# Kernel optimization log

Hardware: AMD Instinct MI355X
Metric: run time of the kernel (lower is better)

Reference implementation:

```python
import jax, jax.numpy as jnp
import numpy as np

N = 8192      # source grid points
M = 8192      # output grid points
NB = 16       # n_basis
WIDTH = 32    # int(n_basis * enhancement)
EPS = 1e-4
LOG2 = 0.6931471805599453


def log_cosh(x):
    a = jnp.abs(x)
    return a + jnp.log1p(jnp.exp(-2.0 * a)) - LOG2


def setup_inputs() -> dict:
    key = jax.random.key(0)
    ks = jax.random.split(key, 9)
    rho = jax.random.uniform(ks[0], (N,), minval=0.05, maxval=2.0)
    gamma = jax.random.uniform(ks[1], (N,), minval=0.01, maxval=1.0)
    coords = jax.random.normal(ks[2], (N, 3)) * 5.0
    weights = jax.random.uniform(ks[3], (N,), minval=0.0, maxval=0.1)
    out_coords = jax.random.normal(ks[4], (M, 3)) * 5.0
    # field_embed params: Linear(1 -> WIDTH), Linear(WIDTH -> NB)
    w1 = jax.random.normal(ks[5], (1, WIDTH)) * 1.0
    b1 = jax.random.normal(ks[6], (WIDTH,)) * 0.1
    w2 = jax.random.normal(ks[7], (WIDTH, NB)) / np.sqrt(WIDTH)
    b2 = jax.random.normal(ks[8], (NB,)) * 0.1
    return {"rho": rho, "gamma": gamma, "coords": coords, "weights": weights,
            "out_coords": out_coords, "w1": w1, "b1": b1, "w2": w2, "b2": b2}


def _field_embed(x, w1, b1, w2, b2):
    # x: (..., 1) -> (..., NB)
    return jnp.tanh(x @ w1 + b1) @ w2 + b2


def reference(rho, gamma, coords, weights, out_coords, w1, b1, w2, b2):
    # rescaled (reduced) density gradient s^2 = gamma / (4 (3 pi^2)^{2/3} rho^{8/3})
    s2 = gamma / (4.0 * (3.0 * jnp.pi ** 2) ** (2.0 / 3.0) * rho ** (8.0 / 3.0))
    x = jnp.log(s2 + EPS)[:, None]                     # (N, 1)
    exponent = log_cosh(_field_embed(x, w1, b1, w2, b2))  # (N, NB)
    heg_scale = log_cosh(_field_embed(jnp.zeros((1, 1), rho.dtype), w1, b1, w2, b2)) ** 1.5  # (1, NB)
    beta = jnp.pi * (rho[:, None] / 2.0) ** (2.0 / 3.0) * exponent  # (N, NB)
    wrho = weights * rho                                # (N,)

    # all-pairs squared distances (M, N), computed once
    d2 = (jnp.sum(out_coords ** 2, axis=1)[:, None]
          + jnp.sum(coords ** 2, axis=1)[None, :]
          - 2.0 * out_coords @ coords.T)
    d2 = jnp.maximum(d2, 0.0)

    # KeOps Genred: y[i, b] = sum_j exp(-beta[j, b] * d2[i, j]) * wrho[j]
    # scan over the (small, fixed) basis axis so only one (M, N) kernel slice lives at a time
    def body(carry, beta_b):                            # beta_b: (N,)
        yb = jnp.exp(-d2 * beta_b[None, :]) @ wrho      # (M,)
        return carry, yb

    _, ys = jax.lax.scan(body, 0, beta.T)               # (NB, M)
    return ys.T * heg_scale                             # (M, NB)
```

## Files before the change

kernel.cpp:

```cpp
#include <hip/hip_runtime.h>
#include <hip/hip_bf16.h>


#define N_PTS 8192
#define M_PTS 8192
#define NBASIS 16
#define WIDTH 32

__device__ __forceinline__ float exp2_hw(float x) { return __builtin_amdgcn_exp2f(x); }
__device__ __forceinline__ float log2_hw(float x) { return __builtin_amdgcn_logf(x); }

__device__ __forceinline__ float fast_tanh(float z) {
    float a = fabsf(z);
    float t = __expf(-2.0f * a);
    float r = (1.0f - t) / (1.0f + t);
    return copysignf(r, z);
}

__device__ __forceinline__ float log_cosh_f(float x) {
    float a = fabsf(x);
    return a + __logf(1.0f + __expf(-2.0f * a)) - 0.6931471805599453f;
}

__global__ __launch_bounds__(64)
void cg_prep(const float* __restrict__ rho,
             const float* __restrict__ gamma,
             const float* __restrict__ coords,
             const float* __restrict__ weights,
             const float* __restrict__ w1,
             const float* __restrict__ b1,
             const float* __restrict__ w2,
             const float* __restrict__ b2,
             float4* __restrict__ cw,
             float4* __restrict__ bnq,
             float* __restrict__ hegf)
{
    const float PI_F = 3.14159265358979323846f;
    const float LOG2E = 1.4426950408889634f;

    __shared__ float s_w1[WIDTH], s_b1[WIDTH], s_w2[WIDTH * NBASIS], s_b2[NBASIS];
    int t = threadIdx.x;
    if (t < WIDTH) { s_w1[t] = w1[t]; s_b1[t] = b1[t]; }
    if (t < NBASIS) s_b2[t] = b2[t];
    #pragma unroll
    for (int k = 0; k < 8; ++k) s_w2[t + 64 * k] = w2[t + 64 * k];
    __syncthreads();

    int j = blockIdx.x * 64 + t;
    {
        float r = rho[j];
        float g = gamma[j];
        const float c83 = 38.28312007948569f;
        float r83 = exp2_hw(2.6666666667f * log2_hw(r));
        float s2 = g / (c83 * r83);
        float x = __logf(s2 + 1e-4f);

        float emb[NBASIS];
        #pragma unroll
        for (int b = 0; b < NBASIS; ++b) emb[b] = s_b2[b];
        #pragma unroll 4
        for (int w = 0; w < WIDTH; ++w) {
            float h = fast_tanh(fmaf(x, s_w1[w], s_b1[w]));
            #pragma unroll
            for (int b = 0; b < NBASIS; ++b)
                emb[b] = fmaf(h, s_w2[w * NBASIS + b], emb[b]);
        }
        float pref = PI_F * exp2_hw(0.6666666667f * log2_hw(0.5f * r));
        float scale = -LOG2E * pref;
        #pragma unroll
        for (int q = 0; q < 4; ++q) {
            bnq[q * N_PTS + j] = make_float4(scale * log_cosh_f(emb[4 * q + 0]),
                                             scale * log_cosh_f(emb[4 * q + 1]),
                                             scale * log_cosh_f(emb[4 * q + 2]),
                                             scale * log_cosh_f(emb[4 * q + 3]));
        }

        cw[j] = make_float4(coords[j * 3 + 0],
                            coords[j * 3 + 1],
                            coords[j * 3 + 2],
                            weights[j] * r);
    }

    if (blockIdx.x == 0 && t == 0) {
        float emb0[NBASIS];
        #pragma unroll
        for (int b = 0; b < NBASIS; ++b) emb0[b] = s_b2[b];
        for (int w = 0; w < WIDTH; ++w) {
            float h = fast_tanh(s_b1[w]);
            #pragma unroll
            for (int b = 0; b < NBASIS; ++b)
                emb0[b] = fmaf(h, s_w2[w * NBASIS + b], emb0[b]);
        }
        #pragma unroll
        for (int b = 0; b < NBASIS; ++b) {
            float lc = fmaxf(log_cosh_f(emb0[b]), 0.0f);
            hegf[b] = lc * sqrtf(lc);
        }
    }
}

__global__ __launch_bounds__(256, 4)
void cg_pairs(const float* __restrict__ oc,
              const float4* __restrict__ cw,
              const float4* __restrict__ bnq,
              const float* __restrict__ hegf,
              float* __restrict__ out)
{
    int wid  = (blockIdx.x << 2) | (threadIdx.x >> 6);
    int lane = threadIdx.x & 63;
    int pair = wid >> 1;
    int half = wid & 1;
    int i0 = pair << 1;
    int i1 = i0 | 1;
    int jbase = half << 12;

    float ox0 = oc[i0 * 3 + 0], oy0 = oc[i0 * 3 + 1], oz0 = oc[i0 * 3 + 2];
    float ox1 = oc[i1 * 3 + 0], oy1 = oc[i1 * 3 + 1], oz1 = oc[i1 * 3 + 2];

    float acc0[NBASIS], acc1[NBASIS];
    #pragma unroll
    for (int b = 0; b < NBASIS; ++b) { acc0[b] = 0.0f; acc1[b] = 0.0f; }

    #pragma unroll 2
    for (int k = 0; k < 64; ++k) {
        int j = jbase + (k << 6) + lane;
        float4 c = cw[j];
        float dx0 = ox0 - c.x, dy0 = oy0 - c.y, dz0 = oz0 - c.z;
        float dx1 = ox1 - c.x, dy1 = oy1 - c.y, dz1 = oz1 - c.z;
        float d20 = fmaf(dx0, dx0, fmaf(dy0, dy0, dz0 * dz0));
        float d21 = fmaf(dx1, dx1, fmaf(dy1, dy1, dz1 * dz1));
        #pragma unroll
        for (int q = 0; q < 4; ++q) {
            float4 b4 = bnq[q * N_PTS + j];
            float e00 = exp2_hw(b4.x * d20);
            float e01 = exp2_hw(b4.y * d20);
            float e02 = exp2_hw(b4.z * d20);
            float e03 = exp2_hw(b4.w * d20);
            float e10 = exp2_hw(b4.x * d21);
            float e11 = exp2_hw(b4.y * d21);
            float e12 = exp2_hw(b4.z * d21);
            float e13 = exp2_hw(b4.w * d21);
            acc0[q * 4 + 0] = fmaf(e00, c.w, acc0[q * 4 + 0]);
            acc0[q * 4 + 1] = fmaf(e01, c.w, acc0[q * 4 + 1]);
            acc0[q * 4 + 2] = fmaf(e02, c.w, acc0[q * 4 + 2]);
            acc0[q * 4 + 3] = fmaf(e03, c.w, acc0[q * 4 + 3]);
            acc1[q * 4 + 0] = fmaf(e10, c.w, acc1[q * 4 + 0]);
            acc1[q * 4 + 1] = fmaf(e11, c.w, acc1[q * 4 + 1]);
            acc1[q * 4 + 2] = fmaf(e12, c.w, acc1[q * 4 + 2]);
            acc1[q * 4 + 3] = fmaf(e13, c.w, acc1[q * 4 + 3]);
        }
    }

    #pragma unroll
    for (int m = 1; m < 64; m <<= 1) {
        #pragma unroll
        for (int b = 0; b < NBASIS; ++b) {
            acc0[b] += __shfl_xor(acc0[b], m, 64);
            acc1[b] += __shfl_xor(acc1[b], m, 64);
        }
    }

    if (lane == 0) {
        #pragma unroll
        for (int b = 0; b < NBASIS; ++b) {
            float h = hegf[b];
            atomicAdd(&out[i0 * NBASIS + b], acc0[b] * h);
            atomicAdd(&out[i1 * NBASIS + b], acc1[b] * h);
        }
    }
}

extern "C" void kernel_launch(void* const* d_in, const int* in_sizes, int n_in,
                              void* d_out, int out_size, void* d_ws, size_t ws_size,
                              hipStream_t stream) {
    const float* rho        = (const float*)d_in[0];
    const float* gamma      = (const float*)d_in[1];
    const float* coords     = (const float*)d_in[2];
    const float* weights    = (const float*)d_in[3];
    const float* out_coords = (const float*)d_in[4];
    const float* w1         = (const float*)d_in[5];
    const float* b1         = (const float*)d_in[6];
    const float* w2         = (const float*)d_in[7];
    const float* b2         = (const float*)d_in[8];

    char* ws = (char*)d_ws;
    float4* cw   = (float4*)(ws);
    float4* bnq  = (float4*)(ws + (128 << 10));
    float*  hegf = (float*) (ws + (640 << 10));

    (void)hipMemsetAsync(d_out, 0, (size_t)M_PTS * NBASIS * sizeof(float), stream);

    cg_prep<<<N_PTS / 64, 64, 0, stream>>>(rho, gamma, coords, weights,
                                           w1, b1, w2, b2,
                                           cw, bnq, hegf);

    cg_pairs<<<M_PTS / 4, 256, 0, stream>>>(out_coords, cw, bnq, hegf,
                                            (float*)d_out);
}
```

Measured before the change: 235.0 us.

## Give each wave the full source range and vectorize pair math with packed floats

Each wave now covers all 8192 source points for its two output rows instead of splitting them across two waves. This lets the results be written with plain stores, so the atomics and the output memset go away. The distance, multiply and accumulate math uses two-wide float vectors so the compiler can emit packed FP32 instructions, while exp2 stays scalar. The grid is halved, which lowers wave-level parallelism (1024 blocks on the device) and doubles the serial loop length per wave.

Result: faster. 190.6 us (-18.9%).

```diff
diff --git a/kernel.cpp b/kernel.cpp
--- a/kernel.cpp
+++ b/kernel.cpp
@@ -6,6 +6,8 @@
 #define M_PTS 8192
 #define NBASIS 16
 #define WIDTH 32
+
+typedef float v2f __attribute__((ext_vector_type(2)));
 
 __device__ __forceinline__ float exp2_hw(float x) { return __builtin_amdgcn_exp2f(x); }
 __device__ __forceinline__ float log2_hw(float x) { return __builtin_amdgcn_logf(x); }
@@ -106,48 +108,42 @@
               const float* __restrict__ hegf,
               float* __restrict__ out)
 {
-    int wid  = (blockIdx.x << 2) | (threadIdx.x >> 6);
+    int wave = (blockIdx.x << 2) | (threadIdx.x >> 6);
     int lane = threadIdx.x & 63;
-    int pair = wid >> 1;
-    int half = wid & 1;
-    int i0 = pair << 1;
+    int i0 = wave << 1;
     int i1 = i0 | 1;
-    int jbase = half << 12;
 
-    float ox0 = oc[i0 * 3 + 0], oy0 = oc[i0 * 3 + 1], oz0 = oc[i0 * 3 + 2];
-    float ox1 = oc[i1 * 3 + 0], oy1 = oc[i1 * 3 + 1], oz1 = oc[i1 * 3 + 2];
+    v2f oxv = { oc[i0 * 3 + 0], oc[i1 * 3 + 0] };
+    v2f oyv = { oc[i0 * 3 + 1], oc[i1 * 3 + 1] };
+    v2f ozv = { oc[i0 * 3 + 2], oc[i1 * 3 + 2] };
 
-    float acc0[NBASIS], acc1[NBASIS];
+    v2f acc[NBASIS];
     #pragma unroll
-    for (int b = 0; b < NBASIS; ++b) { acc0[b] = 0.0f; acc1[b] = 0.0f; }
+    for (int b = 0; b < NBASIS; ++b) acc[b] = (v2f)0.0f;
 
     #pragma unroll 2
-    for (int k = 0; k < 64; ++k) {
-        int j = jbase + (k << 6) + lane;
+    for (int k = 0; k < N_PTS / 64; ++k) {
+        int j = (k << 6) | lane;
         float4 c = cw[j];
-        float dx0 = ox0 - c.x, dy0 = oy0 - c.y, dz0 = oz0 - c.z;
-        float dx1 = ox1 - c.x, dy1 = oy1 - c.y, dz1 = oz1 - c.z;
-        float d20 = fmaf(dx0, dx0, fmaf(dy0, dy0, dz0 * dz0));
-        float d21 = fmaf(dx1, dx1, fmaf(dy1, dy1, dz1 * dz1));
+        v2f dx = oxv - c.x;
+        v2f dy = oyv - c.y;
+        v2f dz = ozv - c.z;
+        v2f d2 = dx * dx + dy * dy + dz * dz;
         #pragma unroll
         for (int q = 0; q < 4; ++q) {
             float4 b4 = bnq[q * N_PTS + j];
-            float e00 = exp2_hw(b4.x * d20);
-            float e01 = exp2_hw(b4.y * d20);
-            float e02 = exp2_hw(b4.z * d20);
-            float e03 = exp2_hw(b4.w * d20);
-            float e10 = exp2_hw(b4.x * d21);
-            float e11 = exp2_hw(b4.y * d21);
-            float e12 = exp2_hw(b4.z * d21);
-            float e13 = exp2_hw(b4.w * d21);
-            acc0[q * 4 + 0] = fmaf(e00, c.w, acc0[q * 4 + 0]);
-            acc0[q * 4 + 1] = fmaf(e01, c.w, acc0[q * 4 + 1]);
-            acc0[q * 4 + 2] = fmaf(e02, c.w, acc0[q * 4 + 2]);
-            acc0[q * 4 + 3] = fmaf(e03, c.w, acc0[q * 4 + 3]);
-            acc1[q * 4 + 0] = fmaf(e10, c.w, acc1[q * 4 + 0]);
-            acc1[q * 4 + 1] = fmaf(e11, c.w, acc1[q * 4 + 1]);
-            acc1[q * 4 + 2] = fmaf(e12, c.w, acc1[q * 4 + 2]);
-            acc1[q * 4 + 3] = fmaf(e13, c.w, acc1[q * 4 + 3]);
+            v2f p0 = b4.x * d2;
+            v2f p1 = b4.y * d2;
+            v2f p2 = b4.z * d2;
+            v2f p3 = b4.w * d2;
+            v2f e0 = { exp2_hw(p0.x), exp2_hw(p0.y) };
+            v2f e1 = { exp2_hw(p1.x), exp2_hw(p1.y) };
+            v2f e2 = { exp2_hw(p2.x), exp2_hw(p2.y) };
+            v2f e3 = { exp2_hw(p3.x), exp2_hw(p3.y) };
+            acc[q * 4 + 0] += e0 * c.w;
+            acc[q * 4 + 1] += e1 * c.w;
+            acc[q * 4 + 2] += e2 * c.w;
+            acc[q * 4 + 3] += e3 * c.w;
         }
     }
 
@@ -155,8 +151,9 @@
     for (int m = 1; m < 64; m <<= 1) {
         #pragma unroll
         for (int b = 0; b < NBASIS; ++b) {
-            acc0[b] += __shfl_xor(acc0[b], m, 64);
-            acc1[b] += __shfl_xor(acc1[b], m, 64);
+            v2f other = { __shfl_xor(acc[b].x, m, 64),
+                          __shfl_xor(acc[b].y, m, 64) };
+            acc[b] += other;
         }
     }
 
@@ -164,8 +161,8 @@
         #pragma unroll
         for (int b = 0; b < NBASIS; ++b) {
             float h = hegf[b];
-            atomicAdd(&out[i0 * NBASIS + b], acc0[b] * h);
-            atomicAdd(&out[i1 * NBASIS + b], acc1[b] * h);
+            out[i0 * NBASIS + b] = acc[b].x * h;
+            out[i1 * NBASIS + b] = acc[b].y * h;
         }
     }
 }
@@ -188,12 +185,10 @@
     float4* bnq  = (float4*)(ws + (128 << 10));
     float*  hegf = (float*) (ws + (640 << 10));
 
-    (void)hipMemsetAsync(d_out, 0, (size_t)M_PTS * NBASIS * sizeof(float), stream);
-
     cg_prep<<<N_PTS / 64, 64, 0, stream>>>(rho, gamma, coords, weights,
                                            w1, b1, w2, b2,
                                            cw, bnq, hegf);
 
-    cg_pairs<<<M_PTS / 4, 256, 0, stream>>>(out_coords, cw, bnq, hegf,
+    cg_pairs<<<M_PTS / 8, 256, 0, stream>>>(out_coords, cw, bnq, hegf,
                                             (float*)d_out);
 }
```
